# Optimization experiments

Measured on AMD Instinct MI355X. Metric: run time of the kernel, lower is better.

## Reference

```python
import jax, jax.numpy as jnp
import numpy as np

BLOCK_K = 128  # per_1x128 block quantization: block_n=1 (per row), block_k=128


def _dequant(wq, scale):
    # wq: [E, N, K] quantized codes; scale: [E, N, ceil(K/BLOCK_K)]
    K = wq.shape[-1]
    s_full = jnp.repeat(scale, BLOCK_K, axis=-1)[..., :K]
    return wq * s_full


def setup_inputs() -> dict:
    key = jax.random.key(0)
    ks = jax.random.split(key, 6)
    T, E, H, I = 1024, 8, 1024, 768
    x = jax.random.normal(ks[0], (T, H), dtype=jnp.float32)
    router_logits = jax.random.normal(ks[1], (T, E), dtype=jnp.float32)
    # fp8 codes simulated as float values; block scales positive (scale_inv)
    w13_weight = jax.random.normal(ks[2], (E, 2 * I, H), dtype=jnp.float32) * 0.05
    w13_weight_scale_inv = jax.random.uniform(ks[3], (E, 2 * I, H // BLOCK_K), dtype=jnp.float32, minval=0.5, maxval=1.5)
    w2_weight = jax.random.normal(ks[4], (E, H, I), dtype=jnp.float32) * 0.05
    w2_weight_scale_inv = jax.random.uniform(ks[5], (E, H, I // BLOCK_K), dtype=jnp.float32, minval=0.5, maxval=1.5)
    return {
        "x": x,
        "router_logits": router_logits,
        "w13_weight": w13_weight,
        "w13_weight_scale_inv": w13_weight_scale_inv,
        "w2_weight": w2_weight,
        "w2_weight_scale_inv": w2_weight_scale_inv,
        "top_k": 2,
    }


def reference(x, router_logits, w13_weight, w13_weight_scale_inv, w2_weight, w2_weight_scale_inv, top_k):
    T, H = x.shape
    E = router_logits.shape[-1]
    I = w2_weight.shape[-1]

    # ---- dequantize block-scaled weights (inline dequant of fp8 grouped GEMM) ----
    w13 = _dequant(w13_weight, w13_weight_scale_inv)   # [E, 2I, H]
    w2 = _dequant(w2_weight, w2_weight_scale_inv)      # [E, H, I]

    # ---- routing: softmax scoring, top_k, renormalize ----
    probs = jax.nn.softmax(router_logits, axis=-1)     # [T, E]
    topk_w, topk_idx = jax.lax.top_k(probs, top_k)     # [T, K]
    topk_w = topk_w / jnp.sum(topk_w, axis=-1, keepdims=True)  # renormalize=True
    # dense combine weights [T, E] (scatter of top_k routing weights)
    combine = jnp.zeros((T, E), x.dtype).at[jnp.arange(T)[:, None], topk_idx].add(topk_w)

    # ---- grouped expert FFN (dense-over-experts reference) ----
    gate_up = jnp.einsum('th,enh->ten', x, w13)        # [T, E, 2I]
    gate, up = gate_up[..., :I], gate_up[..., I:]
    act = jax.nn.silu(gate) * up                       # silu activation ('silu')
    out_e = jnp.einsum('tei,ehi->teh', act, w2)        # [T, E, H]

    # ---- combine ----
    return jnp.einsum('teh,te->th', out_e, combine)    # [T, H]
```

## Files before the change

### kernel.cpp

```cpp
#include <hip/hip_runtime.h>

#define T_TOK 1024
#define H_DIM 1024
#define I_DIM 768
#define E_NUM 8

#define A_W13 6144
#define A_X   512
#define A_Z   512
#define G13 1572864
#define G2   786432

#define GEMM1_BLOCKS 1536
#define W2DQ_BLOCKS  3072

#define SLOT 24576
#define A_OFF 16384

typedef __bf16 bf16x8 __attribute__((ext_vector_type(8)));
typedef float  f32x4  __attribute__((ext_vector_type(4)));

__device__ inline bf16x8 cvt8(float4 a, float4 b, float s) {
    bf16x8 o;
    o[0] = (__bf16)(a.x * s); o[1] = (__bf16)(a.y * s);
    o[2] = (__bf16)(a.z * s); o[3] = (__bf16)(a.w * s);
    o[4] = (__bf16)(b.x * s); o[5] = (__bf16)(b.y * s);
    o[6] = (__bf16)(b.z * s); o[7] = (__bf16)(b.w * s);
    return o;
}

__device__ inline void async16(const void* g, void* l) {
    __builtin_amdgcn_global_load_lds(
        (const __attribute__((address_space(1))) unsigned int*)g,
        (__attribute__((address_space(3))) unsigned int*)l, 16, 0, 0);
}

#define VM_WAIT6  asm volatile("s_waitcnt vmcnt(6)"  ::: "memory")
#define VM_WAIT0  asm volatile("s_waitcnt vmcnt(0)"  ::: "memory")

__global__ __launch_bounds__(256) void prep13_kernel(
    const float* __restrict__ w13, const float* __restrict__ w13s,
    const float* __restrict__ x,   float4* __restrict__ out4,
    __bf16* __restrict__ w13d,     __bf16* __restrict__ xbf,
    const float* __restrict__ logits,
    int* __restrict__ counts, int* __restrict__ base,
    int* __restrict__ tok_list, float* __restrict__ wt_list)
{
    const int bx = blockIdx.x;
    if (bx < A_W13) {
        int g = bx * 256 + threadIdx.x;
        int k8 = g & 127;
        int row = g >> 7;
        float s = w13s[(row << 3) | (k8 >> 4)];
        const float4* src = (const float4*)w13 + (size_t)g * 2;
        *(bf16x8*)(w13d + (size_t)g * 8) = cvt8(src[0], src[1], s);
        return;
    }
    if (bx < A_W13 + A_X) {
        int g = (bx - A_W13) * 256 + threadIdx.x;
        const float4* src = (const float4*)x + (size_t)g * 2;
        *(bf16x8*)(xbf + (size_t)g * 8) = cvt8(src[0], src[1], 1.0f);
        return;
    }
    if (bx < A_W13 + A_X + A_Z) {
        int go = (bx - A_W13 - A_X) * 256 + threadIdx.x;
        float4 z = make_float4(0.f, 0.f, 0.f, 0.f);
        out4[2 * go] = z; out4[2 * go + 1] = z;
        return;
    }
    __shared__ int cnt[E_NUM];
    const int t0 = threadIdx.x;
    if (t0 < E_NUM) cnt[t0] = 0;
    __syncthreads();
#pragma unroll
    for (int tt = 0; tt < 4; tt++) {
        int t = t0 + tt * 256;
        float l[E_NUM];
#pragma unroll
        for (int e = 0; e < E_NUM; e++) l[e] = logits[t * E_NUM + e];
        int e0 = 0; float m0 = l[0];
#pragma unroll
        for (int e = 1; e < E_NUM; e++) if (l[e] > m0) { m0 = l[e]; e0 = e; }
        int e1 = -1; float m1 = -3e38f;
#pragma unroll
        for (int e = 0; e < E_NUM; e++) if (e != e0 && l[e] > m1) { m1 = l[e]; e1 = e; }
        float w0 = 1.0f / (1.0f + expf(m1 - m0));
        float w1 = 1.0f - w0;
        int p0 = atomicAdd(&cnt[e0], 1);
        tok_list[e0 * T_TOK + p0] = t;
        wt_list[e0 * T_TOK + p0] = w0;
        int p1 = atomicAdd(&cnt[e1], 1);
        tok_list[e1 * T_TOK + p1] = t;
        wt_list[e1 * T_TOK + p1] = w1;
    }
    __syncthreads();
    if (t0 == 0) {
        int s = 0;
        for (int e = 0; e < E_NUM; e++) { base[e] = s; counts[e] = cnt[e]; s += cnt[e]; }
    }
}

#define MFMA(A, B, C) __builtin_amdgcn_mfma_f32_16x16x32_bf16(A, B, C, 0, 0, 0)

struct StgEnt { const char* p; int l; };

__global__ __launch_bounds__(256, 3) void gemm1_kernel(
    const __bf16* __restrict__ xbf,
    const __bf16* __restrict__ w13d,
    const int* __restrict__ counts,
    const int* __restrict__ base,
    const int* __restrict__ tok_list,
    __bf16* __restrict__ act,
    const float* __restrict__ w2,
    const float* __restrict__ w2s,
    __bf16* __restrict__ w2d)
{
    const int bx = blockIdx.x;
    if (bx >= GEMM1_BLOCKS) {
        int g2 = (bx - GEMM1_BLOCKS) * 256 + threadIdx.x;
        unsigned row = (unsigned)g2 / 96u;
        int k8 = g2 - row * 96;
        float s = w2s[row * 6 + (k8 >> 4)];
        const float4* src = (const float4*)w2 + (size_t)g2 * 2;
        *(bf16x8*)(w2d + (size_t)g2 * 8) = cvt8(src[0], src[1], s);
        return;
    }

    const int xcd = bx & 7, t = bx >> 3;
    const int p = t % 12, m = t / 12;
    const int P = xcd + 8 * p;
    const int nb = P % 12, e = P / 12;
    const int count = counts[e];
    const int m0 = m * 64;
    if (m0 >= count) return;
    const int n0 = nb * 64;
    const int abase = base[e];

    __shared__ union { uint4 r4[2 * SLOT / 16]; float gu[64 * 132]; } u;
    __shared__ int tokS[64];
    char* ring = (char*)u.r4;

    const int tid = threadIdx.x;
    if (tid < 64) {
        int r = m0 + tid;
        tokS[tid] = (r < count) ? tok_list[e * T_TOK + r] : tok_list[e * T_TOK];
    }
    __syncthreads();

    const int wv = tid >> 6, ln = tid & 63;
    StgEnt se[6];
#pragma unroll
    for (int j = 0; j < 6; j++) {
        int off = wv * 6144 + j * 1024 + ln * 16;
        se[j].l = wv * 6144 + j * 1024;
        if (off < A_OFF) {
            int r = off >> 7, sl = (off >> 4) & 7, g = sl ^ (r & 7);
            int nB = (r < 64) ? (n0 + r) : (I_DIM + n0 + r - 64);
            se[j].p = (const char*)w13d + ((size_t)e * 2 * I_DIM + nB) * 2048 + g * 16;
        } else {
            int ao = off - A_OFF, r = ao >> 7, sl = (ao >> 4) & 7, g = sl ^ (r & 7);
            se[j].p = (const char*)xbf + (size_t)tokS[r] * 2048 + g * 16;
        }
    }

#define ISSUE(kc, sb) do { \
        async16(se[0].p + (kc) * 128, (sb) + se[0].l); \
        async16(se[1].p + (kc) * 128, (sb) + se[1].l); \
        async16(se[2].p + (kc) * 128, (sb) + se[2].l); \
        async16(se[3].p + (kc) * 128, (sb) + se[3].l); \
        async16(se[4].p + (kc) * 128, (sb) + se[4].l); \
        async16(se[5].p + (kc) * 128, (sb) + se[5].l); } while (0)

    const int wid = wv, lane = ln, lrow = lane & 15, quad = lane >> 4;
    int aoff[2][4], boff[2][2];
#pragma unroll
    for (int kk = 0; kk < 2; kk++) {
        int gph = ((kk * 4 + quad) ^ (lrow & 7)) << 4;
#pragma unroll
        for (int i = 0; i < 4; i++) aoff[kk][i] = (i * 16 + lrow) * 128 + gph;
#pragma unroll
        for (int j = 0; j < 2; j++) boff[kk][j] = (wid * 32 + j * 16 + lrow) * 128 + gph;
    }

    f32x4 acc[4][2];
#pragma unroll
    for (int i = 0; i < 4; i++)
#pragma unroll
        for (int j = 0; j < 2; j++) { f32x4 z = {0.f, 0.f, 0.f, 0.f}; acc[i][j] = z; }

    auto compute = [&](const char* sb) {
        const char* Bb = sb;
        const char* Ab = sb + A_OFF;
#pragma unroll
        for (int kk = 0; kk < 2; kk++) {
            bf16x8 b0 = *(const bf16x8*)(Bb + boff[kk][0]);
            bf16x8 b1 = *(const bf16x8*)(Bb + boff[kk][1]);
#pragma unroll
            for (int i = 0; i < 4; i++) {
                bf16x8 a = *(const bf16x8*)(Ab + aoff[kk][i]);
                acc[i][0] = MFMA(a, b0, acc[i][0]);
                acc[i][1] = MFMA(a, b1, acc[i][1]);
            }
        }
    };

    VM_WAIT0;
    ISSUE(0, ring);
#pragma unroll
    for (int k = 0; k < 16; k++) {
        if (k + 1 < 16) ISSUE(k + 1, ring + ((k + 1) & 1) * SLOT);
        if (k < 15) { VM_WAIT6; } else { VM_WAIT0; }
        __builtin_amdgcn_s_barrier();
        compute(ring + (k & 1) * SLOT);
        __builtin_amdgcn_s_barrier();
    }
#undef ISSUE

#pragma unroll
    for (int i = 0; i < 4; i++)
#pragma unroll
        for (int j = 0; j < 2; j++)
#pragma unroll
            for (int r = 0; r < 4; r++) {
                int mr = i * 16 + quad * 4 + r;
                int c = wid * 32 + j * 16 + lrow;
                u.gu[mr * 132 + c] = acc[i][j][r];
            }
    __syncthreads();

#pragma unroll
    for (int ii = 0; ii < 16; ii++) {
        int o = ii * 256 + tid;
        int mr = o >> 6, c = o & 63;
        if (m0 + mr < count) {
            float g  = u.gu[mr * 132 + c];
            float up = u.gu[mr * 132 + 64 + c];
            float a  = g / (1.0f + expf(-g)) * up;
            act[(size_t)(abase + m0 + mr) * I_DIM + n0 + c] = (__bf16)a;
        }
    }
}

__global__ __launch_bounds__(256, 3) void gemm2_kernel(
    const __bf16* __restrict__ act,
    const __bf16* __restrict__ w2d,
    const int* __restrict__ counts,
    const int* __restrict__ base,
    const int* __restrict__ tok_list,
    const float* __restrict__ wt_list,
    float* __restrict__ out)
{
    const int bx = blockIdx.x;
    const int xcd = bx & 7, t = bx >> 3;
    const int p = t & 7, m = t >> 3;
    const int P = xcd + 8 * p;
    const int nb = P & 7, e = P >> 3;
    const int count = counts[e];
    const int m0 = m * 64;
    if (m0 >= count) return;
    const int n0 = nb * 128;
    const int abase = base[e];

    __shared__ uint4 r4[2 * SLOT / 16];
    char* ring = (char*)r4;

    const int tid = threadIdx.x;
    const int wv = tid >> 6, ln = tid & 63;

    StgEnt se[6];
#pragma unroll
    for (int j = 0; j < 6; j++) {
        int off = wv * 6144 + j * 1024 + ln * 16;
        se[j].l = wv * 6144 + j * 1024;
        if (off < A_OFF) {
            int r = off >> 7, sl = (off >> 4) & 7, g = sl ^ (r & 7);
            se[j].p = (const char*)w2d + ((size_t)e * H_DIM + n0 + r) * 1536 + g * 16;
        } else {
            int ao = off - A_OFF, r = ao >> 7, sl = (ao >> 4) & 7, g = sl ^ (r & 7);
            int gr = abase + m0 + r; if (gr > 2 * T_TOK - 1) gr = 2 * T_TOK - 1;
            se[j].p = (const char*)act + (size_t)gr * 1536 + g * 16;
        }
    }

#define ISSUE(kc, sb) do { \
        async16(se[0].p + (kc) * 128, (sb) + se[0].l); \
        async16(se[1].p + (kc) * 128, (sb) + se[1].l); \
        async16(se[2].p + (kc) * 128, (sb) + se[2].l); \
        async16(se[3].p + (kc) * 128, (sb) + se[3].l); \
        async16(se[4].p + (kc) * 128, (sb) + se[4].l); \
        async16(se[5].p + (kc) * 128, (sb) + se[5].l); } while (0)

    const int wid = wv, lane = ln, lrow = lane & 15, quad = lane >> 4;
    int aoff[2][4], boff[2][2];
#pragma unroll
    for (int kk = 0; kk < 2; kk++) {
        int gph = ((kk * 4 + quad) ^ (lrow & 7)) << 4;
#pragma unroll
        for (int i = 0; i < 4; i++) aoff[kk][i] = (i * 16 + lrow) * 128 + gph;
#pragma unroll
        for (int j = 0; j < 2; j++) boff[kk][j] = (wid * 32 + j * 16 + lrow) * 128 + gph;
    }

    f32x4 acc[4][2];
#pragma unroll
    for (int i = 0; i < 4; i++)
#pragma unroll
        for (int j = 0; j < 2; j++) { f32x4 z = {0.f, 0.f, 0.f, 0.f}; acc[i][j] = z; }

    auto compute = [&](const char* sb) {
        const char* Bb = sb;
        const char* Ab = sb + A_OFF;
#pragma unroll
        for (int kk = 0; kk < 2; kk++) {
            bf16x8 b0 = *(const bf16x8*)(Bb + boff[kk][0]);
            bf16x8 b1 = *(const bf16x8*)(Bb + boff[kk][1]);
#pragma unroll
            for (int i = 0; i < 4; i++) {
                bf16x8 a = *(const bf16x8*)(Ab + aoff[kk][i]);
                acc[i][0] = MFMA(a, b0, acc[i][0]);
                acc[i][1] = MFMA(a, b1, acc[i][1]);
            }
        }
    };

    VM_WAIT0;
    ISSUE(0, ring);
#pragma unroll
    for (int k = 0; k < 12; k++) {
        if (k + 1 < 12) ISSUE(k + 1, ring + ((k + 1) & 1) * SLOT);
        if (k < 11) { VM_WAIT6; } else { VM_WAIT0; }
        __builtin_amdgcn_s_barrier();
        compute(ring + (k & 1) * SLOT);
        __builtin_amdgcn_s_barrier();
    }
#undef ISSUE

#pragma unroll
    for (int i = 0; i < 4; i++)
#pragma unroll
        for (int r = 0; r < 4; r++) {
            int mr = i * 16 + quad * 4 + r;
            if (m0 + mr < count) {
                int   tk = tok_list[e * T_TOK + m0 + mr];
                float w  = wt_list[e * T_TOK + m0 + mr];
#pragma unroll
                for (int j = 0; j < 2; j++) {
                    int h = n0 + wid * 32 + j * 16 + lrow;
                    atomicAdd(&out[(size_t)tk * H_DIM + h], w * acc[i][j][r]);
                }
            }
        }
}

extern "C" void kernel_launch(void* const* d_in, const int* in_sizes, int n_in,
                              void* d_out, int out_size, void* d_ws, size_t ws_size,
                              hipStream_t stream) {
    (void)in_sizes; (void)n_in; (void)out_size; (void)ws_size;
    const float* x      = (const float*)d_in[0];
    const float* logits = (const float*)d_in[1];
    const float* w13    = (const float*)d_in[2];
    const float* w13s   = (const float*)d_in[3];
    const float* w2     = (const float*)d_in[4];
    const float* w2s    = (const float*)d_in[5];
    float* out = (float*)d_out;

    char* ws = (char*)d_ws;
    int*    counts   = (int*)ws;
    int*    base     = (int*)(ws + 128);
    int*    tok_list = (int*)(ws + 256);
    float*  wt_list  = (float*)(ws + 256 + 32768);
    __bf16* act      = (__bf16*)(ws + 65792);
    __bf16* xbf      = (__bf16*)(ws + 65792 + 3145728);
    __bf16* w13d     = (__bf16*)(ws + 65792 + 3145728 + 2097152);
    __bf16* w2d      = (__bf16*)(ws + 65792 + 3145728 + 2097152 + 25165824);

    prep13_kernel<<<dim3(A_W13 + A_X + A_Z + 1), 256, 0, stream>>>(
        w13, w13s, x, (float4*)out, w13d, xbf,
        logits, counts, base, tok_list, wt_list);
    gemm1_kernel<<<dim3(GEMM1_BLOCKS + W2DQ_BLOCKS), 256, 0, stream>>>(
        xbf, w13d, counts, base, tok_list, act, w2, w2s, w2d);
    gemm2_kernel<<<dim3(1024), 256, 0, stream>>>(
        act, w2d, counts, base, tok_list, wt_list, out);
}
```

Baseline: 151.1 us.

## Merge dequant and both GEMMs into one persistent work-queue kernel with dependency counters

Replaces the three-kernel pipeline with a light prep kernel plus a persistent kernel. Its 768 blocks pull work items from an atomic queue: w13 dequant slices, output zeroing, w2 dequant, GEMM1 strips and GEMM2 tiles. Per-item counters and spin-waits enforce dependencies, so dequant of one expert/N tile overlaps GEMMs on others and launch boundaries go away. The cost is spin-wait stalls, atomic traffic and fences, and deadlock risk if a waiting block's producers cannot get scheduled.

```diff
diff --git a/kernel.cpp b/kernel.cpp
--- a/kernel.cpp
+++ b/kernel.cpp
@@ -5,17 +5,25 @@
 #define I_DIM 768
 #define E_NUM 8
 
-#define A_W13 6144
-#define A_X   512
-#define A_Z   512
-#define G13 1572864
-#define G2   786432
-
-#define GEMM1_BLOCKS 1536
-#define W2DQ_BLOCKS  3072
+#define NWORK 768
+#define N_ILV 2304
+#define N_ZERO 64
+#define N_W2DQ 384
+#define N_G2   1024
+#define Q_ZERO N_ILV
+#define Q_W2DQ (N_ILV + N_ZERO)
+#define Q_G2   (N_ILV + N_ZERO + N_W2DQ)
+#define NITEMS (N_ILV + N_ZERO + N_W2DQ + N_G2)
 
 #define SLOT 24576
 #define A_OFF 16384
+
+#define C_QHEAD 0
+#define C_ZCNT  16
+#define C_W2CNT 32
+#define C_PAIR(P)  (48 + (P) * 16)
+#define C_STRIP(s) (1584 + (s) * 16)
+#define C_TOTAL 3632
 
 typedef __bf16 bf16x8 __attribute__((ext_vector_type(8)));
 typedef float  f32x4  __attribute__((ext_vector_type(4)));
@@ -37,39 +45,27 @@
 
 #define VM_WAIT6  asm volatile("s_waitcnt vmcnt(6)"  ::: "memory")
 #define VM_WAIT0  asm volatile("s_waitcnt vmcnt(0)"  ::: "memory")
-
-__global__ __launch_bounds__(256) void prep13_kernel(
-    const float* __restrict__ w13, const float* __restrict__ w13s,
-    const float* __restrict__ x,   float4* __restrict__ out4,
-    __bf16* __restrict__ w13d,     __bf16* __restrict__ xbf,
-    const float* __restrict__ logits,
+#define MFMA(A, B, C) __builtin_amdgcn_mfma_f32_16x16x32_bf16(A, B, C, 0, 0, 0)
+
+struct StgEnt { const char* p; int l; };
+
+__global__ __launch_bounds__(256) void prep_lite(
+    const float* __restrict__ x, const float* __restrict__ logits,
+    __bf16* __restrict__ xbf,
     int* __restrict__ counts, int* __restrict__ base,
-    int* __restrict__ tok_list, float* __restrict__ wt_list)
+    int* __restrict__ tok_list, float* __restrict__ wt_list,
+    int* __restrict__ ctrl)
 {
     const int bx = blockIdx.x;
-    if (bx < A_W13) {
+    if (bx < 512) {
         int g = bx * 256 + threadIdx.x;
-        int k8 = g & 127;
-        int row = g >> 7;
-        float s = w13s[(row << 3) | (k8 >> 4)];
-        const float4* src = (const float4*)w13 + (size_t)g * 2;
-        *(bf16x8*)(w13d + (size_t)g * 8) = cvt8(src[0], src[1], s);
-        return;
-    }
-    if (bx < A_W13 + A_X) {
-        int g = (bx - A_W13) * 256 + threadIdx.x;
         const float4* src = (const float4*)x + (size_t)g * 2;
         *(bf16x8*)(xbf + (size_t)g * 8) = cvt8(src[0], src[1], 1.0f);
         return;
     }
-    if (bx < A_W13 + A_X + A_Z) {
-        int go = (bx - A_W13 - A_X) * 256 + threadIdx.x;
-        float4 z = make_float4(0.f, 0.f, 0.f, 0.f);
-        out4[2 * go] = z; out4[2 * go + 1] = z;
-        return;
-    }
+    const int t0 = threadIdx.x;
+    for (int i = t0; i < C_TOTAL; i += 256) ctrl[i] = 0;
     __shared__ int cnt[E_NUM];
-    const int t0 = threadIdx.x;
     if (t0 < E_NUM) cnt[t0] = 0;
     __syncthreads();
 #pragma unroll
@@ -100,70 +96,84 @@
     }
 }
 
-#define MFMA(A, B, C) __builtin_amdgcn_mfma_f32_16x16x32_bf16(A, B, C, 0, 0, 0)
-
-struct StgEnt { const char* p; int l; };
-
-__global__ __launch_bounds__(256, 3) void gemm1_kernel(
+__global__ __launch_bounds__(256, 3) void moe_queue(
+    const float* __restrict__ w13, const float* __restrict__ w13s,
+    const float* __restrict__ w2,  const float* __restrict__ w2s,
     const __bf16* __restrict__ xbf,
-    const __bf16* __restrict__ w13d,
-    const int* __restrict__ counts,
-    const int* __restrict__ base,
-    const int* __restrict__ tok_list,
-    __bf16* __restrict__ act,
-    const float* __restrict__ w2,
-    const float* __restrict__ w2s,
-    __bf16* __restrict__ w2d)
+    __bf16* __restrict__ w13d, __bf16* __restrict__ w2d,
+    const int* __restrict__ counts, const int* __restrict__ base,
+    const int* __restrict__ tok_list, const float* __restrict__ wt_list,
+    __bf16* __restrict__ act, float* __restrict__ out,
+    int* __restrict__ ctrl)
 {
-    const int bx = blockIdx.x;
-    if (bx >= GEMM1_BLOCKS) {
-        int g2 = (bx - GEMM1_BLOCKS) * 256 + threadIdx.x;
-        unsigned row = (unsigned)g2 / 96u;
-        int k8 = g2 - row * 96;
-        float s = w2s[row * 6 + (k8 >> 4)];
-        const float4* src = (const float4*)w2 + (size_t)g2 * 2;
-        *(bf16x8*)(w2d + (size_t)g2 * 8) = cvt8(src[0], src[1], s);
-        return;
-    }
-
-    const int xcd = bx & 7, t = bx >> 3;
-    const int p = t % 12, m = t / 12;
-    const int P = xcd + 8 * p;
-    const int nb = P % 12, e = P / 12;
-    const int count = counts[e];
-    const int m0 = m * 64;
-    if (m0 >= count) return;
-    const int n0 = nb * 64;
-    const int abase = base[e];
-
     __shared__ union { uint4 r4[2 * SLOT / 16]; float gu[64 * 132]; } u;
     __shared__ int tokS[64];
+    __shared__ int curs;
     char* ring = (char*)u.r4;
-
     const int tid = threadIdx.x;
-    if (tid < 64) {
-        int r = m0 + tid;
-        tokS[tid] = (r < count) ? tok_list[e * T_TOK + r] : tok_list[e * T_TOK];
-    }
-    __syncthreads();
-
-    const int wv = tid >> 6, ln = tid & 63;
-    StgEnt se[6];
-#pragma unroll
-    for (int j = 0; j < 6; j++) {
-        int off = wv * 6144 + j * 1024 + ln * 16;
-        se[j].l = wv * 6144 + j * 1024;
-        if (off < A_OFF) {
-            int r = off >> 7, sl = (off >> 4) & 7, g = sl ^ (r & 7);
-            int nB = (r < 64) ? (n0 + r) : (I_DIM + n0 + r - 64);
-            se[j].p = (const char*)w13d + ((size_t)e * 2 * I_DIM + nB) * 2048 + g * 16;
-        } else {
-            int ao = off - A_OFF, r = ao >> 7, sl = (ao >> 4) & 7, g = sl ^ (r & 7);
-            se[j].p = (const char*)xbf + (size_t)tokS[r] * 2048 + g * 16;
-        }
-    }
-
-#define ISSUE(kc, sb) do { \
+
+    for (;;) {
+        __syncthreads();
+        if (tid == 0) curs = atomicAdd(&ctrl[C_QHEAD], 1);
+        __syncthreads();
+        const int item = curs;
+        if (item >= NITEMS) return;
+
+        if (item < N_ILV) {
+            const int P = item / 24, s = item % 24;
+            const int e = P / 12, nb = P % 12;
+            if (s < 8) {
+                const int n0rel = (s < 4) ? (nb * 64 + s * 16)
+                                          : (I_DIM + nb * 64 + (s - 4) * 16);
+                const size_t gb = (size_t)(e * 1536 + n0rel) * 128;
+#pragma unroll
+                for (int k = 0; k < 8; k++) {
+                    size_t g = gb + k * 256 + tid;
+                    int row = (int)(g >> 7), k8 = (int)(g & 127);
+                    float sc = w13s[(row << 3) | (k8 >> 4)];
+                    const float4* src = (const float4*)w13 + g * 2;
+                    *(bf16x8*)(w13d + g * 8) = cvt8(src[0], src[1], sc);
+                }
+                __threadfence(); __syncthreads();
+                if (tid == 0) atomicAdd(&ctrl[C_PAIR(P)], 1);
+            } else {
+                const int m = s - 8;
+                const int count = counts[e];
+                const int m0 = m * 64;
+                if (m0 < count) {
+                    const int n0 = nb * 64;
+                    const int abase = base[e];
+                    if (tid == 0) {
+                        while (atomicAdd(&ctrl[C_PAIR(P)], 0) < 8)
+                            __builtin_amdgcn_s_sleep(2);
+                    }
+                    __syncthreads();
+                    __threadfence();
+
+                    if (tid < 64) {
+                        int r = m0 + tid;
+                        tokS[tid] = (r < count) ? tok_list[e * T_TOK + r]
+                                                : tok_list[e * T_TOK];
+                    }
+                    __syncthreads();
+
+                    const int wv = tid >> 6, ln = tid & 63;
+                    StgEnt se[6];
+#pragma unroll
+                    for (int j = 0; j < 6; j++) {
+                        int off = wv * 6144 + j * 1024 + ln * 16;
+                        se[j].l = wv * 6144 + j * 1024;
+                        if (off < A_OFF) {
+                            int r = off >> 7, sl = (off >> 4) & 7, g = sl ^ (r & 7);
+                            int nB = (r < 64) ? (n0 + r) : (I_DIM + n0 + r - 64);
+                            se[j].p = (const char*)w13d + ((size_t)e * 2 * I_DIM + nB) * 2048 + g * 16;
+                        } else {
+                            int ao = off - A_OFF, r = ao >> 7, sl = (ao >> 4) & 7, g = sl ^ (r & 7);
+                            se[j].p = (const char*)xbf + (size_t)tokS[r] * 2048 + g * 16;
+                        }
+                    }
+
+#define ISSUE1(kc, sb) do { \
         async16(se[0].p + (kc) * 128, (sb) + se[0].l); \
         async16(se[1].p + (kc) * 128, (sb) + se[1].l); \
         async16(se[2].p + (kc) * 128, (sb) + se[2].l); \
@@ -171,118 +181,138 @@
         async16(se[4].p + (kc) * 128, (sb) + se[4].l); \
         async16(se[5].p + (kc) * 128, (sb) + se[5].l); } while (0)
 
-    const int wid = wv, lane = ln, lrow = lane & 15, quad = lane >> 4;
-    int aoff[2][4], boff[2][2];
-#pragma unroll
-    for (int kk = 0; kk < 2; kk++) {
-        int gph = ((kk * 4 + quad) ^ (lrow & 7)) << 4;
-#pragma unroll
-        for (int i = 0; i < 4; i++) aoff[kk][i] = (i * 16 + lrow) * 128 + gph;
-#pragma unroll
-        for (int j = 0; j < 2; j++) boff[kk][j] = (wid * 32 + j * 16 + lrow) * 128 + gph;
-    }
-
-    f32x4 acc[4][2];
-#pragma unroll
-    for (int i = 0; i < 4; i++)
-#pragma unroll
-        for (int j = 0; j < 2; j++) { f32x4 z = {0.f, 0.f, 0.f, 0.f}; acc[i][j] = z; }
-
-    auto compute = [&](const char* sb) {
-        const char* Bb = sb;
-        const char* Ab = sb + A_OFF;
-#pragma unroll
-        for (int kk = 0; kk < 2; kk++) {
-            bf16x8 b0 = *(const bf16x8*)(Bb + boff[kk][0]);
-            bf16x8 b1 = *(const bf16x8*)(Bb + boff[kk][1]);
-#pragma unroll
-            for (int i = 0; i < 4; i++) {
-                bf16x8 a = *(const bf16x8*)(Ab + aoff[kk][i]);
-                acc[i][0] = MFMA(a, b0, acc[i][0]);
-                acc[i][1] = MFMA(a, b1, acc[i][1]);
+                    const int wid = wv, lane = ln, lrow = lane & 15, quad = lane >> 4;
+                    int aoff[2][4], boff[2][2];
+#pragma unroll
+                    for (int kk = 0; kk < 2; kk++) {
+                        int gph = ((kk * 4 + quad) ^ (lrow & 7)) << 4;
+#pragma unroll
+                        for (int i = 0; i < 4; i++) aoff[kk][i] = (i * 16 + lrow) * 128 + gph;
+#pragma unroll
+                        for (int j = 0; j < 2; j++) boff[kk][j] = (wid * 32 + j * 16 + lrow) * 128 + gph;
+                    }
+
+                    f32x4 acc[4][2];
+#pragma unroll
+                    for (int i = 0; i < 4; i++)
+#pragma unroll
+                        for (int j = 0; j < 2; j++) { f32x4 z = {0.f, 0.f, 0.f, 0.f}; acc[i][j] = z; }
+
+                    auto compute = [&](const char* sb) {
+                        const char* Bb = sb;
+                        const char* Ab = sb + A_OFF;
+#pragma unroll
+                        for (int kk = 0; kk < 2; kk++) {
+                            bf16x8 b0 = *(const bf16x8*)(Bb + boff[kk][0]);
+                            bf16x8 b1 = *(const bf16x8*)(Bb + boff[kk][1]);
+#pragma unroll
+                            for (int i = 0; i < 4; i++) {
+                                bf16x8 a = *(const bf16x8*)(Ab + aoff[kk][i]);
+                                acc[i][0] = MFMA(a, b0, acc[i][0]);
+                                acc[i][1] = MFMA(a, b1, acc[i][1]);
+                            }
+                        }
+                    };
+
+                    VM_WAIT0;
+                    ISSUE1(0, ring);
+#pragma unroll
+                    for (int k = 0; k < 16; k++) {
+                        if (k + 1 < 16) ISSUE1(k + 1, ring + ((k + 1) & 1) * SLOT);
+                        if (k < 15) { VM_WAIT6; } else { VM_WAIT0; }
+                        __builtin_amdgcn_s_barrier();
+                        compute(ring + (k & 1) * SLOT);
+                        __builtin_amdgcn_s_barrier();
+                    }
+#undef ISSUE1
+
+#pragma unroll
+                    for (int i = 0; i < 4; i++)
+#pragma unroll
+                        for (int j = 0; j < 2; j++)
+#pragma unroll
+                            for (int r = 0; r < 4; r++) {
+                                int mr = i * 16 + quad * 4 + r;
+                                int c = wid * 32 + j * 16 + lrow;
+                                u.gu[mr * 132 + c] = acc[i][j][r];
+                            }
+                    __syncthreads();
+
+#pragma unroll
+                    for (int ii = 0; ii < 16; ii++) {
+                        int o = ii * 256 + tid;
+                        int mr = o >> 6, c = o & 63;
+                        if (m0 + mr < count) {
+                            float g  = u.gu[mr * 132 + c];
+                            float up = u.gu[mr * 132 + 64 + c];
+                            float a  = g / (1.0f + expf(-g)) * up;
+                            act[(size_t)(abase + m0 + mr) * I_DIM + n0 + c] = (__bf16)a;
+                        }
+                    }
+                    __threadfence(); __syncthreads();
+                    if (tid == 0) atomicAdd(&ctrl[C_STRIP(e * 16 + m)], 1);
+                }
             }
-        }
-    };
-
-    VM_WAIT0;
-    ISSUE(0, ring);
-#pragma unroll
-    for (int k = 0; k < 16; k++) {
-        if (k + 1 < 16) ISSUE(k + 1, ring + ((k + 1) & 1) * SLOT);
-        if (k < 15) { VM_WAIT6; } else { VM_WAIT0; }
-        __builtin_amdgcn_s_barrier();
-        compute(ring + (k & 1) * SLOT);
-        __builtin_amdgcn_s_barrier();
-    }
-#undef ISSUE
-
-#pragma unroll
-    for (int i = 0; i < 4; i++)
-#pragma unroll
-        for (int j = 0; j < 2; j++)
-#pragma unroll
-            for (int r = 0; r < 4; r++) {
-                int mr = i * 16 + quad * 4 + r;
-                int c = wid * 32 + j * 16 + lrow;
-                u.gu[mr * 132 + c] = acc[i][j][r];
+        } else if (item < Q_W2DQ) {
+            float4* out4 = (float4*)out;
+            float4 z = make_float4(0.f, 0.f, 0.f, 0.f);
+            const int zi = item - Q_ZERO;
+#pragma unroll
+            for (int k = 0; k < 8; k++) {
+                size_t go = (size_t)zi * 2048 + k * 256 + tid;
+                out4[2 * go] = z; out4[2 * go + 1] = z;
             }
-    __syncthreads();
-
-#pragma unroll
-    for (int ii = 0; ii < 16; ii++) {
-        int o = ii * 256 + tid;
-        int mr = o >> 6, c = o & 63;
-        if (m0 + mr < count) {
-            float g  = u.gu[mr * 132 + c];
-            float up = u.gu[mr * 132 + 64 + c];
-            float a  = g / (1.0f + expf(-g)) * up;
-            act[(size_t)(abase + m0 + mr) * I_DIM + n0 + c] = (__bf16)a;
-        }
-    }
-}
-
-__global__ __launch_bounds__(256, 3) void gemm2_kernel(
-    const __bf16* __restrict__ act,
-    const __bf16* __restrict__ w2d,
-    const int* __restrict__ counts,
-    const int* __restrict__ base,
-    const int* __restrict__ tok_list,
-    const float* __restrict__ wt_list,
-    float* __restrict__ out)
-{
-    const int bx = blockIdx.x;
-    const int xcd = bx & 7, t = bx >> 3;
-    const int p = t & 7, m = t >> 3;
-    const int P = xcd + 8 * p;
-    const int nb = P & 7, e = P >> 3;
-    const int count = counts[e];
-    const int m0 = m * 64;
-    if (m0 >= count) return;
-    const int n0 = nb * 128;
-    const int abase = base[e];
-
-    __shared__ uint4 r4[2 * SLOT / 16];
-    char* ring = (char*)r4;
-
-    const int tid = threadIdx.x;
-    const int wv = tid >> 6, ln = tid & 63;
-
-    StgEnt se[6];
-#pragma unroll
-    for (int j = 0; j < 6; j++) {
-        int off = wv * 6144 + j * 1024 + ln * 16;
-        se[j].l = wv * 6144 + j * 1024;
-        if (off < A_OFF) {
-            int r = off >> 7, sl = (off >> 4) & 7, g = sl ^ (r & 7);
-            se[j].p = (const char*)w2d + ((size_t)e * H_DIM + n0 + r) * 1536 + g * 16;
+            __threadfence(); __syncthreads();
+            if (tid == 0) atomicAdd(&ctrl[C_ZCNT], 1);
+        } else if (item < Q_G2) {
+            const int q = item - Q_W2DQ;
+#pragma unroll
+            for (int k = 0; k < 8; k++) {
+                int g2 = q * 2048 + k * 256 + tid;
+                unsigned row = (unsigned)g2 / 96u;
+                int k8 = g2 - row * 96;
+                float sc = w2s[row * 6 + (k8 >> 4)];
+                const float4* src = (const float4*)w2 + (size_t)g2 * 2;
+                *(bf16x8*)(w2d + (size_t)g2 * 8) = cvt8(src[0], src[1], sc);
+            }
+            __threadfence(); __syncthreads();
+            if (tid == 0) atomicAdd(&ctrl[C_W2CNT], 1);
         } else {
-            int ao = off - A_OFF, r = ao >> 7, sl = (ao >> 4) & 7, g = sl ^ (r & 7);
-            int gr = abase + m0 + r; if (gr > 2 * T_TOK - 1) gr = 2 * T_TOK - 1;
-            se[j].p = (const char*)act + (size_t)gr * 1536 + g * 16;
-        }
-    }
-
-#define ISSUE(kc, sb) do { \
+            const int idx2 = item - Q_G2;
+            const int xcd = idx2 & 7, t2 = idx2 >> 3;
+            const int p2 = t2 & 7, m = t2 >> 3;
+            const int P2 = xcd + 8 * p2;
+            const int nb = P2 & 7, e = P2 >> 3;
+            const int count = counts[e];
+            const int m0 = m * 64;
+            if (m0 < count) {
+                const int n0 = nb * 128;
+                const int abase = base[e];
+                if (tid == 0) {
+                    while (atomicAdd(&ctrl[C_ZCNT], 0) < N_ZERO)  __builtin_amdgcn_s_sleep(2);
+                    while (atomicAdd(&ctrl[C_W2CNT], 0) < N_W2DQ) __builtin_amdgcn_s_sleep(2);
+                    while (atomicAdd(&ctrl[C_STRIP(e * 16 + m)], 0) < 12) __builtin_amdgcn_s_sleep(2);
+                }
+                __syncthreads();
+                __threadfence();
+
+                const int wv = tid >> 6, ln = tid & 63;
+                StgEnt se[6];
+#pragma unroll
+                for (int j = 0; j < 6; j++) {
+                    int off = wv * 6144 + j * 1024 + ln * 16;
+                    se[j].l = wv * 6144 + j * 1024;
+                    if (off < A_OFF) {
+                        int r = off >> 7, sl = (off >> 4) & 7, g = sl ^ (r & 7);
+                        se[j].p = (const char*)w2d + ((size_t)e * H_DIM + n0 + r) * 1536 + g * 16;
+                    } else {
+                        int ao = off - A_OFF, r = ao >> 7, sl = (ao >> 4) & 7, g = sl ^ (r & 7);
+                        int gr = abase + m0 + r; if (gr > 2 * T_TOK - 1) gr = 2 * T_TOK - 1;
+                        se[j].p = (const char*)act + (size_t)gr * 1536 + g * 16;
+                    }
+                }
+
+#define ISSUE2(kc, sb) do { \
         async16(se[0].p + (kc) * 128, (sb) + se[0].l); \
         async16(se[1].p + (kc) * 128, (sb) + se[1].l); \
         async16(se[2].p + (kc) * 128, (sb) + se[2].l); \
@@ -290,66 +320,69 @@
         async16(se[4].p + (kc) * 128, (sb) + se[4].l); \
         async16(se[5].p + (kc) * 128, (sb) + se[5].l); } while (0)
 
-    const int wid = wv, lane = ln, lrow = lane & 15, quad = lane >> 4;
-    int aoff[2][4], boff[2][2];
-#pragma unroll
-    for (int kk = 0; kk < 2; kk++) {
-        int gph = ((kk * 4 + quad) ^ (lrow & 7)) << 4;
-#pragma unroll
-        for (int i = 0; i < 4; i++) aoff[kk][i] = (i * 16 + lrow) * 128 + gph;
-#pragma unroll
-        for (int j = 0; j < 2; j++) boff[kk][j] = (wid * 32 + j * 16 + lrow) * 128 + gph;
-    }
-
-    f32x4 acc[4][2];
-#pragma unroll
-    for (int i = 0; i < 4; i++)
-#pragma unroll
-        for (int j = 0; j < 2; j++) { f32x4 z = {0.f, 0.f, 0.f, 0.f}; acc[i][j] = z; }
-
-    auto compute = [&](const char* sb) {
-        const char* Bb = sb;
-        const char* Ab = sb + A_OFF;
-#pragma unroll
-        for (int kk = 0; kk < 2; kk++) {
-            bf16x8 b0 = *(const bf16x8*)(Bb + boff[kk][0]);
-            bf16x8 b1 = *(const bf16x8*)(Bb + boff[kk][1]);
-#pragma unroll
-            for (int i = 0; i < 4; i++) {
-                bf16x8 a = *(const bf16x8*)(Ab + aoff[kk][i]);
-                acc[i][0] = MFMA(a, b0, acc[i][0]);
-                acc[i][1] = MFMA(a, b1, acc[i][1]);
+                const int wid = wv, lane = ln, lrow = lane & 15, quad = lane >> 4;
+                int aoff[2][4], boff[2][2];
+#pragma unroll
+                for (int kk = 0; kk < 2; kk++) {
+                    int gph = ((kk * 4 + quad) ^ (lrow & 7)) << 4;
+#pragma unroll
+                    for (int i = 0; i < 4; i++) aoff[kk][i] = (i * 16 + lrow) * 128 + gph;
+#pragma unroll
+                    for (int j = 0; j < 2; j++) boff[kk][j] = (wid * 32 + j * 16 + lrow) * 128 + gph;
+                }
+
+                f32x4 acc[4][2];
+#pragma unroll
+                for (int i = 0; i < 4; i++)
+#pragma unroll
+                    for (int j = 0; j < 2; j++) { f32x4 z = {0.f, 0.f, 0.f, 0.f}; acc[i][j] = z; }
+
+                auto compute2 = [&](const char* sb) {
+                    const char* Bb = sb;
+                    const char* Ab = sb + A_OFF;
+#pragma unroll
+                    for (int kk = 0; kk < 2; kk++) {
+                        bf16x8 b0 = *(const bf16x8*)(Bb + boff[kk][0]);
+                        bf16x8 b1 = *(const bf16x8*)(Bb + boff[kk][1]);
+#pragma unroll
+                        for (int i = 0; i < 4; i++) {
+                            bf16x8 a = *(const bf16x8*)(Ab + aoff[kk][i]);
+                            acc[i][0] = MFMA(a, b0, acc[i][0]);
+                            acc[i][1] = MFMA(a, b1, acc[i][1]);
+                        }
+                    }
+                };
+
+                VM_WAIT0;
+                ISSUE2(0, ring);
+#pragma unroll
+                for (int k = 0; k < 12; k++) {
+                    if (k + 1 < 12) ISSUE2(k + 1, ring + ((k + 1) & 1) * SLOT);
+                    if (k < 11) { VM_WAIT6; } else { VM_WAIT0; }
+                    __builtin_amdgcn_s_barrier();
+                    compute2(ring + (k & 1) * SLOT);
+                    __builtin_amdgcn_s_barrier();
+                }
+#undef ISSUE2
+
+#pragma unroll
+                for (int i = 0; i < 4; i++)
+#pragma unroll
+                    for (int r = 0; r < 4; r++) {
+                        int mr = i * 16 + quad * 4 + r;
+                        if (m0 + mr < count) {
+                            int   tk = tok_list[e * T_TOK + m0 + mr];
+                            float w  = wt_list[e * T_TOK + m0 + mr];
+#pragma unroll
+                            for (int j = 0; j < 2; j++) {
+                                int h = n0 + wid * 32 + j * 16 + lrow;
+                                atomicAdd(&out[(size_t)tk * H_DIM + h], w * acc[i][j][r]);
+                            }
+                        }
+                    }
             }
         }
-    };
-
-    VM_WAIT0;
-    ISSUE(0, ring);
-#pragma unroll
-    for (int k = 0; k < 12; k++) {
-        if (k + 1 < 12) ISSUE(k + 1, ring + ((k + 1) & 1) * SLOT);
-        if (k < 11) { VM_WAIT6; } else { VM_WAIT0; }
-        __builtin_amdgcn_s_barrier();
-        compute(ring + (k & 1) * SLOT);
-        __builtin_amdgcn_s_barrier();
     }
-#undef ISSUE
-
-#pragma unroll
-    for (int i = 0; i < 4; i++)
-#pragma unroll
-        for (int r = 0; r < 4; r++) {
-            int mr = i * 16 + quad * 4 + r;
-            if (m0 + mr < count) {
-                int   tk = tok_list[e * T_TOK + m0 + mr];
-                float w  = wt_list[e * T_TOK + m0 + mr];
-#pragma unroll
-                for (int j = 0; j < 2; j++) {
-                    int h = n0 + wid * 32 + j * 16 + lrow;
-                    atomicAdd(&out[(size_t)tk * H_DIM + h], w * acc[i][j][r]);
-                }
-            }
-        }
 }
 
 extern "C" void kernel_launch(void* const* d_in, const int* in_sizes, int n_in,
@@ -373,12 +406,11 @@
     __bf16* xbf      = (__bf16*)(ws + 65792 + 3145728);
     __bf16* w13d     = (__bf16*)(ws + 65792 + 3145728 + 2097152);
     __bf16* w2d      = (__bf16*)(ws + 65792 + 3145728 + 2097152 + 25165824);
-
-    prep13_kernel<<<dim3(A_W13 + A_X + A_Z + 1), 256, 0, stream>>>(
-        w13, w13s, x, (float4*)out, w13d, xbf,
-        logits, counts, base, tok_list, wt_list);
-    gemm1_kernel<<<dim3(GEMM1_BLOCKS + W2DQ_BLOCKS), 256, 0, stream>>>(
-        xbf, w13d, counts, base, tok_list, act, w2, w2s, w2d);
-    gemm2_kernel<<<dim3(1024), 256, 0, stream>>>(
-        act, w2d, counts, base, tok_list, wt_list, out);
+    int*    ctrl     = (int*)(ws + 43057408);
+
+    prep_lite<<<dim3(513), 256, 0, stream>>>(
+        x, logits, xbf, counts, base, tok_list, wt_list, ctrl);
+    moe_queue<<<dim3(NWORK), 256, 0, stream>>>(
+        w13, w13s, w2, w2s, xbf, w13d, w2d,
+        counts, base, tok_list, wt_list, act, out, ctrl);
 }
```

New measurement: 525.5 us. +247.7%, slower.

## Split gemm2 K dimension in two and move output zeroing into gemm1 launch

Applied to the files above, without the earlier changes.

Gemm2 now launches twice as many blocks, and each block handles half of the I=768 reduction (6 k-chunks instead of 12). Partial sums are combined through the existing atomicAdd into the output. This raises parallelism for the second grouped GEMM, at the cost of doubling the atomic traffic to the output. Zeroing of the output moves from the prep kernel to extra blocks in the gemm1 launch, which keeps the prep kernel smaller and still runs before gemm2.

```diff
diff --git a/kernel.cpp b/kernel.cpp
--- a/kernel.cpp
+++ b/kernel.cpp
@@ -7,12 +7,12 @@
 
 #define A_W13 6144
 #define A_X   512
-#define A_Z   512
 #define G13 1572864
 #define G2   786432
 
 #define GEMM1_BLOCKS 1536
 #define W2DQ_BLOCKS  3072
+#define ZERO_BLOCKS  128
 
 #define SLOT 24576
 #define A_OFF 16384
@@ -40,7 +40,7 @@
 
 __global__ __launch_bounds__(256) void prep13_kernel(
     const float* __restrict__ w13, const float* __restrict__ w13s,
-    const float* __restrict__ x,   float4* __restrict__ out4,
+    const float* __restrict__ x,
     __bf16* __restrict__ w13d,     __bf16* __restrict__ xbf,
     const float* __restrict__ logits,
     int* __restrict__ counts, int* __restrict__ base,
@@ -62,12 +62,6 @@
         *(bf16x8*)(xbf + (size_t)g * 8) = cvt8(src[0], src[1], 1.0f);
         return;
     }
-    if (bx < A_W13 + A_X + A_Z) {
-        int go = (bx - A_W13 - A_X) * 256 + threadIdx.x;
-        float4 z = make_float4(0.f, 0.f, 0.f, 0.f);
-        out4[2 * go] = z; out4[2 * go + 1] = z;
-        return;
-    }
     __shared__ int cnt[E_NUM];
     const int t0 = threadIdx.x;
     if (t0 < E_NUM) cnt[t0] = 0;
@@ -113,9 +107,18 @@
     __bf16* __restrict__ act,
     const float* __restrict__ w2,
     const float* __restrict__ w2s,
-    __bf16* __restrict__ w2d)
+    __bf16* __restrict__ w2d,
+    float4* __restrict__ out4)
 {
     const int bx = blockIdx.x;
+    if (bx >= GEMM1_BLOCKS + W2DQ_BLOCKS) {
+        int zi = bx - (GEMM1_BLOCKS + W2DQ_BLOCKS);
+        float4 z = make_float4(0.f, 0.f, 0.f, 0.f);
+#pragma unroll
+        for (int k = 0; k < 8; k++)
+            out4[zi * 2048 + k * 256 + threadIdx.x] = z;
+        return;
+    }
     if (bx >= GEMM1_BLOCKS) {
         int g2 = (bx - GEMM1_BLOCKS) * 256 + threadIdx.x;
         unsigned row = (unsigned)g2 / 96u;
@@ -251,7 +254,9 @@
     float* __restrict__ out)
 {
     const int bx = blockIdx.x;
-    const int xcd = bx & 7, t = bx >> 3;
+    const int h = bx >> 10;
+    const int v = bx & 1023;
+    const int xcd = v & 7, t = v >> 3;
     const int p = t & 7, m = t >> 3;
     const int P = xcd + 8 * p;
     const int nb = P & 7, e = P >> 3;
@@ -280,6 +285,7 @@
             int gr = abase + m0 + r; if (gr > 2 * T_TOK - 1) gr = 2 * T_TOK - 1;
             se[j].p = (const char*)act + (size_t)gr * 1536 + g * 16;
         }
+        se[j].p += h * 768;
     }
 
 #define ISSUE(kc, sb) do { \
@@ -326,9 +332,9 @@
     VM_WAIT0;
     ISSUE(0, ring);
 #pragma unroll
-    for (int k = 0; k < 12; k++) {
-        if (k + 1 < 12) ISSUE(k + 1, ring + ((k + 1) & 1) * SLOT);
-        if (k < 11) { VM_WAIT6; } else { VM_WAIT0; }
+    for (int k = 0; k < 6; k++) {
+        if (k + 1 < 6) ISSUE(k + 1, ring + ((k + 1) & 1) * SLOT);
+        if (k < 5) { VM_WAIT6; } else { VM_WAIT0; }
         __builtin_amdgcn_s_barrier();
         compute(ring + (k & 1) * SLOT);
         __builtin_amdgcn_s_barrier();
@@ -345,8 +351,8 @@
                 float w  = wt_list[e * T_TOK + m0 + mr];
 #pragma unroll
                 for (int j = 0; j < 2; j++) {
-                    int h = n0 + wid * 32 + j * 16 + lrow;
-                    atomicAdd(&out[(size_t)tk * H_DIM + h], w * acc[i][j][r]);
+                    int hh = n0 + wid * 32 + j * 16 + lrow;
+                    atomicAdd(&out[(size_t)tk * H_DIM + hh], w * acc[i][j][r]);
                 }
             }
         }
@@ -374,11 +380,11 @@
     __bf16* w13d     = (__bf16*)(ws + 65792 + 3145728 + 2097152);
     __bf16* w2d      = (__bf16*)(ws + 65792 + 3145728 + 2097152 + 25165824);
 
-    prep13_kernel<<<dim3(A_W13 + A_X + A_Z + 1), 256, 0, stream>>>(
-        w13, w13s, x, (float4*)out, w13d, xbf,
+    prep13_kernel<<<dim3(A_W13 + A_X + 1), 256, 0, stream>>>(
+        w13, w13s, x, w13d, xbf,
         logits, counts, base, tok_list, wt_list);
-    gemm1_kernel<<<dim3(GEMM1_BLOCKS + W2DQ_BLOCKS), 256, 0, stream>>>(
-        xbf, w13d, counts, base, tok_list, act, w2, w2s, w2d);
-    gemm2_kernel<<<dim3(1024), 256, 0, stream>>>(
+    gemm1_kernel<<<dim3(GEMM1_BLOCKS + W2DQ_BLOCKS + ZERO_BLOCKS), 256, 0, stream>>>(
+        xbf, w13d, counts, base, tok_list, act, w2, w2s, w2d, (float4*)out);
+    gemm2_kernel<<<dim3(2048), 256, 0, stream>>>(
         act, w2d, counts, base, tok_list, wt_list, out);
 }
```

Result: slower. 155.1 us (+2.6%).
